# Performance work log

Measured on AMD Instinct MI355X. Metric: run time of the kernel, lower is better.

Reference implementation:

```python
import jax, jax.numpy as jnp
import numpy as np

EMBED = 1024
HEADS = 16
HEAD_DIM = EMBED // HEADS
WIN = 256  # attention_window w; band width = 2w+1


def setup_inputs() -> dict:
    key = jax.random.key(0)
    ks = jax.random.split(key, 10)
    b, s, e = 2, 4096, EMBED
    scale = 1.0 / np.sqrt(e)
    inp = {"x": jax.random.normal(ks[0], (b, s, e), jnp.float32)}
    for i, (wn, bn) in enumerate([("Wq", "bq"), ("Wk", "bk"), ("Wv", "bv"), ("Wo", "bo")]):
        inp[wn] = jax.random.normal(ks[1 + i], (e, e), jnp.float32) * scale
        inp[bn] = jax.random.normal(ks[5 + i], (e,), jnp.float32) * 0.01
    return inp


def _rope_headaxis(x):
    # Replicates RotaryEmbedding applied to [b, s, h, d]: the original indexes
    # x.shape[2] (== num_heads here), so phase varies over the HEAD axis.
    h, d = x.shape[2], x.shape[3]
    inv = 1.0 / (10000.0 ** (jnp.arange(0, d, 2, dtype=jnp.float32) / d))
    freqs = jnp.arange(h, dtype=jnp.float32)[:, None] * inv[None, :]
    emb = jnp.concatenate([freqs, freqs], axis=-1)  # [h, d]
    cos = jnp.cos(emb)[None, None]  # [1,1,h,d]
    sin = jnp.sin(emb)[None, None]
    x2 = jnp.stack([-x[..., 1::2], x[..., 0::2]], axis=-1).reshape(x.shape)
    return x * cos + x2 * sin


def reference(x, Wq, bq, Wk, bk, Wv, bv, Wo, bo):
    b, s, e = x.shape
    h, d, w = HEADS, HEAD_DIM, WIN
    q = (x @ Wq.T + bq).reshape(b, s, h, d)
    k = (x @ Wk.T + bk).reshape(b, s, h, d)
    v = (x @ Wv.T + bv).reshape(b, s, h, d)
    q = _rope_headaxis(q) / jnp.sqrt(jnp.float32(d))
    k = _rope_headaxis(k)

    # Band (sliding-window) attention: query chunk c of size w attends to key
    # chunks c-1, c, c+1 (3w keys); relative-position + boundary masking makes
    # this identical to the original sliding_chunks band of width 2w+1.
    nc = s // w
    qc = q.reshape(b, nc, w, h, d)
    pad = [(0, 0), (w, w), (0, 0), (0, 0)]
    kp = jnp.pad(k, pad)
    vp = jnp.pad(v, pad)
    idx = jnp.arange(nc)[:, None] * w + jnp.arange(3 * w)[None, :]  # [nc, 3w]
    k3 = kp[:, idx]  # [b, nc, 3w, h, d]
    v3 = vp[:, idx]
    scores = jnp.einsum('bcxhd,bcyhd->bhcxy', qc, k3)  # [b,h,nc,w,3w]

    c = jnp.arange(nc)[:, None, None]
    xq = jnp.arange(w)[None, :, None]
    y = jnp.arange(3 * w)[None, None, :]
    kpos = c * w + y - w  # absolute key position
    valid = (y >= xq) & (y <= xq + 2 * w) & (kpos >= 0) & (kpos < s)
    scores = jnp.where(valid[None, None], scores, -jnp.inf)

    probs = jax.nn.softmax(scores, axis=-1)  # fp32 softmax, as in original
    ctx = jnp.einsum('bhcxy,bcyhd->bcxhd', probs, v3).reshape(b, s, e)
    return ctx @ Wo.T + bo
```

## Files before the change

### kernel.cpp

```cpp
#include <hip/hip_runtime.h>


typedef _Float16 half8 __attribute__((ext_vector_type(8)));
typedef _Float16 half4v __attribute__((ext_vector_type(4)));
typedef float floatx4 __attribute__((ext_vector_type(4)));

typedef __attribute__((address_space(3))) unsigned int lds_u32;
typedef const __attribute__((address_space(1))) unsigned int glb_u32;

__device__ __forceinline__ void async_copy16(const void* g, void* l) {
  __builtin_amdgcn_global_load_lds((glb_u32*)g, (lds_u32*)l, 16, 0, 0);
}

__global__ __launch_bounds__(256) void convert_kernel(
    const float* __restrict__ x, const float* __restrict__ wq,
    const float* __restrict__ wk, const float* __restrict__ wv,
    const float* __restrict__ wo, _Float16* __restrict__ dst) {
  const int e0 = (blockIdx.x * 256 + threadIdx.x) * 4;
  const float* src; int off;
  if      (e0 <  8388608) { src = x;  off = e0; }
  else if (e0 <  9437184) { src = wq; off = e0 -  8388608; }
  else if (e0 < 10485760) { src = wk; off = e0 -  9437184; }
  else if (e0 < 11534336) { src = wv; off = e0 - 10485760; }
  else                    { src = wo; off = e0 - 11534336; }
  const float4 f = *(const float4*)(src + off);
  half4v h;
  h[0] = (_Float16)f.x; h[1] = (_Float16)f.y;
  h[2] = (_Float16)f.z; h[3] = (_Float16)f.w;
  *(half4v*)(dst + e0) = h;
}

__global__ __launch_bounds__(256, 2) void gemm_qkv_kernel(
    const _Float16* __restrict__ A, const _Float16* __restrict__ w0,
    const _Float16* __restrict__ w1, const _Float16* __restrict__ w2,
    const float* __restrict__ b0, const float* __restrict__ b1,
    const float* __restrict__ b2, _Float16* __restrict__ o0,
    _Float16* __restrict__ o1, _Float16* __restrict__ o2) {
  __shared__ _Float16 smem[17408];
  _Float16* As = smem;
  _Float16* Bs = smem + 8192;

  const int tid = threadIdx.x;
  const int w = tid >> 6, lane = tid & 63;
  const int l4 = lane & 15, quad = lane >> 4;
  const int wm = w & 1, wn = w >> 1;

  const int bid = blockIdx.x;
  const int xcd = bid & 7, li = bid >> 3;
  const int z = li >> 6, r_ = li & 63;
  const int n_l = r_ >> 3, m_l = r_ & 7;
  const int m0 = (xcd * 8 + m_l) * 128;
  const int n0 = n_l * 128;

  const _Float16* B; const float* bias; _Float16* out;
  if (z == 0)      { B = w0; bias = b0; out = o0; }
  else if (z == 1) { B = w1; bias = b1; out = o1; }
  else             { B = w2; bias = b2; out = o2; }
  const bool dorope = z < 2;
  const float scl = (z == 0) ? 0.18033688f : 1.0f;

  const floatx4 zero = {0.f, 0.f, 0.f, 0.f};
  floatx4 acc[4][4];
#pragma unroll
  for (int i = 0; i < 4; ++i)
#pragma unroll
    for (int j = 0; j < 4; ++j) acc[i][j] = zero;

  for (int kt = 0; kt < 16; ++kt) {
    const int k0 = kt * 64;
#pragma unroll
    for (int i = 0; i < 4; ++i) {
      const int p = i * 256 + tid;
      const int r = p >> 3;
      const int c = (p & 7) ^ (r & 7);
      async_copy16(A + (m0 + r) * 1024 + k0 + c * 8, As + (i * 256 + w * 64) * 8);
      async_copy16(B + (n0 + r) * 1024 + k0 + c * 8, Bs + (i * 256 + w * 64) * 8);
    }
    __syncthreads();
#pragma unroll
    for (int ks = 0; ks < 2; ++ks) {
      half8 af[4], bf[4];
#pragma unroll
      for (int mt = 0; mt < 4; ++mt)
        af[mt] = *(const half8*)(As + (wm * 64 + mt * 16 + l4) * 64 +
                                 (((ks * 4 + quad) ^ (l4 & 7)) * 8));
#pragma unroll
      for (int nt = 0; nt < 4; ++nt)
        bf[nt] = *(const half8*)(Bs + (wn * 64 + nt * 16 + l4) * 64 +
                                 (((ks * 4 + quad) ^ (l4 & 7)) * 8));
#pragma unroll
      for (int mt = 0; mt < 4; ++mt)
#pragma unroll
        for (int nt = 0; nt < 4; ++nt)
          acc[mt][nt] = __builtin_amdgcn_mfma_f32_16x16x32_f16(af[mt], bf[nt], acc[mt][nt], 0, 0, 0);
    }
    __syncthreads();
  }

  _Float16* tile = smem;
#pragma unroll
  for (int nt = 0; nt < 4; ++nt) {
    const int n = n0 + wn * 64 + nt * 16 + l4;
    const float bval = bias[n];
    const int hh = n >> 6;
    float c_ = 1.f, ss = 0.f;
    if (dorope) {
      const float freq = __expf((float)(n & 31) * -0.28782314f);
      float s_;
      __sincosf((float)hh * freq, &s_, &c_);
      ss = (n & 1) ? s_ : -s_;
    }
#pragma unroll
    for (int mt = 0; mt < 4; ++mt)
#pragma unroll
      for (int r = 0; r < 4; ++r) {
        float val = acc[mt][nt][r] + bval;
        const float prt = __shfl_xor(val, 1);
        if (dorope) val = (val * c_ + prt * ss) * scl;
        const int ml = wm * 64 + mt * 16 + quad * 4 + r;
        const int nl = wn * 64 + nt * 16 + l4;
        if (z == 2) tile[nl * 132 + ml] = (_Float16)val;
        else        tile[ml * 132 + nl] = (_Float16)val;
      }
  }
  __syncthreads();
  if (z == 2) {
#pragma unroll
    for (int j = 0; j < 8; ++j) {
      const int idx = j * 256 + tid;
      const int row = idx >> 4, cb = idx & 15;
      const int n = n0 + row, hh = n >> 6, dd = n & 63;
      const int m = m0 + cb * 8, bb = m >> 12, s = m & 4095;
      const half8 vals = *(const half8*)(tile + row * 132 + cb * 8);
      *(half8*)(out + (bb * 16 + hh) * 262144 + dd * 4096 + s) = vals;
    }
  } else {
#pragma unroll
    for (int j = 0; j < 8; ++j) {
      const int idx = j * 256 + tid;
      const int row = idx >> 4, cb = idx & 15;
      const int n = n0 + cb * 8, hh = n >> 6, dd = n & 63;
      const int m = m0 + row, bb = m >> 12, s = m & 4095;
      const half8 vals = *(const half8*)(tile + row * 132 + cb * 8);
      *(half8*)(out + ((bb * 16 + hh) * 4096 + s) * 64 + dd) = vals;
    }
  }
}

__global__ __launch_bounds__(256, 2) void gemm_out_kernel(
    const _Float16* __restrict__ A, const _Float16* __restrict__ B,
    const float* __restrict__ bias, float* __restrict__ out) {
  __shared__ _Float16 smem[16384];
  _Float16* As = smem;
  _Float16* Bs = smem + 8192;

  const int tid = threadIdx.x;
  const int w = tid >> 6, lane = tid & 63;
  const int l4 = lane & 15, quad = lane >> 4;
  const int wm = w & 1, wn = w >> 1;

  const int bid = blockIdx.x;
  const int xcd = bid & 7, li = bid >> 3;
  const int n_l = li >> 3, m_l = li & 7;
  const int m0 = (xcd * 8 + m_l) * 128;
  const int n0 = n_l * 128;

  const floatx4 zero = {0.f, 0.f, 0.f, 0.f};
  floatx4 acc[4][4];
#pragma unroll
  for (int i = 0; i < 4; ++i)
#pragma unroll
    for (int j = 0; j < 4; ++j) acc[i][j] = zero;

  for (int kt = 0; kt < 16; ++kt) {
    const int k0 = kt * 64;
#pragma unroll
    for (int i = 0; i < 4; ++i) {
      const int p = i * 256 + tid;
      const int r = p >> 3;
      const int c = (p & 7) ^ (r & 7);
      async_copy16(A + (m0 + r) * 1024 + k0 + c * 8, As + (i * 256 + w * 64) * 8);
      async_copy16(B + (n0 + r) * 1024 + k0 + c * 8, Bs + (i * 256 + w * 64) * 8);
    }
    __syncthreads();
#pragma unroll
    for (int ks = 0; ks < 2; ++ks) {
      half8 af[4], bf[4];
#pragma unroll
      for (int mt = 0; mt < 4; ++mt)
        af[mt] = *(const half8*)(As + (wm * 64 + mt * 16 + l4) * 64 +
                                 (((ks * 4 + quad) ^ (l4 & 7)) * 8));
#pragma unroll
      for (int nt = 0; nt < 4; ++nt)
        bf[nt] = *(const half8*)(Bs + (wn * 64 + nt * 16 + l4) * 64 +
                                 (((ks * 4 + quad) ^ (l4 & 7)) * 8));
#pragma unroll
      for (int mt = 0; mt < 4; ++mt)
#pragma unroll
        for (int nt = 0; nt < 4; ++nt)
          acc[mt][nt] = __builtin_amdgcn_mfma_f32_16x16x32_f16(af[mt], bf[nt], acc[mt][nt], 0, 0, 0);
    }
    __syncthreads();
  }

#pragma unroll
  for (int nt = 0; nt < 4; ++nt) {
    const int n = n0 + wn * 64 + nt * 16 + l4;
    const float bval = bias[n];
#pragma unroll
    for (int mt = 0; mt < 4; ++mt)
#pragma unroll
      for (int r = 0; r < 4; ++r) {
        const int m = m0 + wm * 64 + mt * 16 + quad * 4 + r;
        out[m * 1024 + n] = acc[mt][nt][r] + bval;
      }
  }
}

__global__ __launch_bounds__(256, 2) void attn_kernel(
    const _Float16* __restrict__ qg, const _Float16* __restrict__ kg,
    const _Float16* __restrict__ vtg, _Float16* __restrict__ ctx) {
  __shared__ _Float16 Ks[128 * 64];
  __shared__ _Float16 Vs[64 * 128];

  const int tid = threadIdx.x;
  const int w = tid >> 6, lane = tid & 63;
  const int l4 = lane & 15, quad = lane >> 4;
  const int q0 = blockIdx.x * 256;
  const int bh = blockIdx.y;
  const _Float16* qbh = qg + bh * 262144;
  const _Float16* kbh = kg + bh * 262144;
  const _Float16* vbh = vtg + bh * 262144;

  half8 qf[2][2][2];
#pragma unroll
  for (int sub = 0; sub < 2; ++sub)
#pragma unroll
    for (int nt = 0; nt < 2; ++nt)
#pragma unroll
      for (int ks = 0; ks < 2; ++ks)
        qf[sub][nt][ks] = *(const half8*)(qbh + (q0 + sub * 128 + w * 32 + nt * 16 + l4) * 64 +
                                          ks * 32 + quad * 8);

  const floatx4 zero = {0.f, 0.f, 0.f, 0.f};
  floatx4 OT[2][4][2];
  float l_st[2][2];
#pragma unroll
  for (int sub = 0; sub < 2; ++sub) {
#pragma unroll
    for (int md = 0; md < 4; ++md)
#pragma unroll
      for (int nt = 0; nt < 2; ++nt) OT[sub][md][nt] = zero;
#pragma unroll
    for (int nt = 0; nt < 2; ++nt) l_st[sub][nt] = 0.f;
  }

  for (int t = 0; t < 6; ++t) {
    const int kv0 = q0 - 256 + t * 128;
    if (kv0 < 0 || kv0 >= 4096) continue;

#pragma unroll
    for (int i = 0; i < 4; ++i) {
      const int p = i * 256 + tid;
      const int rk = p >> 3, ck = (p & 7) ^ (rk & 7);
      async_copy16(kbh + (kv0 + rk) * 64 + ck * 8, Ks + (i * 256 + w * 64) * 8);
      const int rv = p >> 4, cv = (p & 15) ^ (rv & 7);
      async_copy16(vbh + rv * 4096 + kv0 + cv * 8, Vs + (i * 256 + w * 64) * 8);
    }
    __syncthreads();

#pragma unroll
    for (int sub = 0; sub < 2; ++sub) {
      if ((t == 0 && sub == 1) || (t == 5 && sub == 0)) continue;
      const bool needmask = (t == 0 && sub == 0) || (t == 1 && sub == 1) ||
                            (t == 4 && sub == 0) || (t == 5 && sub == 1);
      const int qbase = q0 + sub * 128 + w * 32;

#pragma unroll
      for (int hf = 0; hf < 2; ++hf) {
        const int kb = hf * 64;

        floatx4 ST[4][2];
#pragma unroll
        for (int m = 0; m < 4; ++m)
#pragma unroll
          for (int nt = 0; nt < 2; ++nt) ST[m][nt] = zero;
#pragma unroll
        for (int ks = 0; ks < 2; ++ks)
#pragma unroll
          for (int m = 0; m < 4; ++m) {
            const half8 kf = *(const half8*)(Ks + (kb + m * 16 + l4) * 64 +
                                             ((ks * 4 + quad) ^ (l4 & 7)) * 8);
#pragma unroll
            for (int nt = 0; nt < 2; ++nt)
              ST[m][nt] = __builtin_amdgcn_mfma_f32_16x16x32_f16(kf, qf[sub][nt][ks], ST[m][nt], 0, 0, 0);
          }

        if (needmask) {
#pragma unroll
          for (int m = 0; m < 4; ++m)
#pragma unroll
            for (int r = 0; r < 4; ++r) {
              const int key = kv0 + kb + m * 16 + quad * 4 + r;
#pragma unroll
              for (int nt = 0; nt < 2; ++nt) {
                const int d = key - (qbase + nt * 16 + l4);
                if (d < -256 || d > 256) ST[m][nt][r] = -1e30f;
              }
            }
        }

#pragma unroll
        for (int nt = 0; nt < 2; ++nt) {
          float rs = 0.f;
#pragma unroll
          for (int m = 0; m < 4; ++m)
#pragma unroll
            for (int r = 0; r < 4; ++r) {
              const float pv = exp2f(ST[m][nt][r] - 4.0f);
              ST[m][nt][r] = pv;
              rs += pv;
            }
          l_st[sub][nt] += rs;
        }

#pragma unroll
        for (int m = 0; m < 4; ++m) {
          half4v pb[2];
#pragma unroll
          for (int nt = 0; nt < 2; ++nt) {
            const auto lo = __builtin_amdgcn_cvt_pkrtz(ST[m][nt][0], ST[m][nt][1]);
            const auto hi = __builtin_amdgcn_cvt_pkrtz(ST[m][nt][2], ST[m][nt][3]);
            pb[nt][0] = (_Float16)lo[0]; pb[nt][1] = (_Float16)lo[1];
            pb[nt][2] = (_Float16)hi[0]; pb[nt][3] = (_Float16)hi[1];
          }
#pragma unroll
          for (int md = 0; md < 4; ++md) {
            const half4v vf = *(const half4v*)(Vs + (md * 16 + l4) * 128 +
                                               (((hf * 8 + m * 2 + (quad >> 1)) ^ (l4 & 7)) * 8 +
                                                (quad & 1) * 4));
#pragma unroll
            for (int nt = 0; nt < 2; ++nt)
              OT[sub][md][nt] = __builtin_amdgcn_mfma_f32_16x16x16f16(vf, pb[nt], OT[sub][md][nt], 0, 0, 0);
          }
        }
      }
    }
    __syncthreads();
  }

  const int b = bh >> 4, hh = bh & 15;
#pragma unroll
  for (int sub = 0; sub < 2; ++sub)
#pragma unroll
    for (int nt = 0; nt < 2; ++nt) {
      float lt = l_st[sub][nt];
      lt += __shfl_xor(lt, 16);
      lt += __shfl_xor(lt, 32);
      const float inv_l = 1.f / lt;
      const int s = q0 + sub * 128 + w * 32 + nt * 16 + l4;
#pragma unroll
      for (int md = 0; md < 4; ++md) {
        half4v o;
#pragma unroll
        for (int r = 0; r < 4; ++r) o[r] = (_Float16)(OT[sub][md][nt][r] * inv_l);
        *(half4v*)(ctx + (b * 4096 + s) * 1024 + hh * 64 + md * 16 + quad * 4) = o;
      }
    }
}

extern "C" void kernel_launch(void* const* d_in, const int* in_sizes, int n_in,
                              void* d_out, int out_size, void* d_ws, size_t ws_size,
                              hipStream_t stream) {
  const float* x  = (const float*)d_in[0];
  const float* Wq = (const float*)d_in[1];
  const float* bq = (const float*)d_in[2];
  const float* Wk = (const float*)d_in[3];
  const float* bk = (const float*)d_in[4];
  const float* Wv = (const float*)d_in[5];
  const float* bv = (const float*)d_in[6];
  const float* Wo = (const float*)d_in[7];
  const float* bo = (const float*)d_in[8];

  _Float16* ws   = (_Float16*)d_ws;
  _Float16* xh   = ws;
  _Float16* wqh  = ws + 8388608;
  _Float16* wkh  = ws + 9437184;
  _Float16* wvh  = ws + 10485760;
  _Float16* woh  = ws + 11534336;
  _Float16* qh   = ws + 12582912;
  _Float16* kh   = ws + 20971520;
  _Float16* vth  = ws + 29360128;
  _Float16* ctxh = xh;

  convert_kernel<<<12288, 256, 0, stream>>>(x, Wq, Wk, Wv, Wo, ws);
  gemm_qkv_kernel<<<1536, 256, 0, stream>>>(xh, wqh, wkh, wvh,
                                            bq, bk, bv, qh, kh, vth);
  attn_kernel<<<dim3(16, 32), 256, 0, stream>>>(qh, kh, vth, ctxh);
  gemm_out_kernel<<<512, 256, 0, stream>>>(ctxh, woh, bo, (float*)d_out);
}
```

Baseline: 232.6 us.

## Use 256x128 GEMM tiles with triple-buffered async loads and split MFMA phases

Replaces both GEMM main loops with a shared routine that computes 256x128 tiles (BK=32) using a three-stage LDS ring of async global->LDS loads, explicit vmcnt waits, and s_setprio around MFMA bursts. Grid sizes halve and each wave accumulates 8x4 fragments, raising arithmetic intensity and overlapping loads with compute. The QKV epilogue is split into two 128-row halves to reuse LDS for the transposed writes. Costs are more registers and LDS (72KB per block), which may limit occupancy, and fewer blocks relative to CU count.

```diff
diff --git a/kernel.cpp b/kernel.cpp
--- a/kernel.cpp
+++ b/kernel.cpp
@@ -30,15 +30,113 @@
   *(half4v*)(dst + e0) = h;
 }
 
+__device__ __forceinline__ void gemm256_mainloop(
+    const _Float16* __restrict__ Ag, const _Float16* __restrict__ Bg,
+    _Float16* smem, const int m0, const int n0, floatx4 (&acc)[8][4]) {
+  const int tid = threadIdx.x;
+  const int w = tid >> 6, lane = tid & 63;
+  const int l4 = lane & 15, quad = lane >> 4;
+  const int wm = w & 1, wn = w >> 1;
+
+  int srcA[4], srcB[2];
+#pragma unroll
+  for (int i = 0; i < 4; ++i) {
+    const int p = i * 256 + tid;
+    const int r = p >> 2;
+    const int g = (p & 3) ^ ((r >> 1) & 3);
+    srcA[i] = (m0 + r) * 1024 + g * 8;
+  }
+#pragma unroll
+  for (int i = 0; i < 2; ++i) {
+    const int p = i * 256 + tid;
+    const int r = p >> 2;
+    const int g = (p & 3) ^ ((r >> 1) & 3);
+    srcB[i] = (n0 + r) * 1024 + g * 8;
+  }
+  const int dstw = w * 512;
+
+  const int swz = (quad ^ ((l4 >> 1) & 3)) * 8;
+  const int a_off = (wm * 128 + l4) * 32 + swz;
+  const int b_off = (wn * 64 + l4) * 32 + swz;
+
+  const floatx4 zero = {0.f, 0.f, 0.f, 0.f};
+#pragma unroll
+  for (int i = 0; i < 8; ++i)
+#pragma unroll
+    for (int j = 0; j < 4; ++j) acc[i][j] = zero;
+
+  auto stage = [&](int bufbase, int kt, int ph) {
+    _Float16* Ad = smem + bufbase;
+    _Float16* Bd = Ad + 8192;
+    const int k0 = kt * 32;
+    if (ph == 0) {
+      async_copy16(Ag + srcA[0] + k0, Ad + dstw);
+      async_copy16(Ag + srcA[1] + k0, Ad + 2048 + dstw);
+      async_copy16(Bg + srcB[0] + k0, Bd + dstw);
+    } else {
+      async_copy16(Ag + srcA[2] + k0, Ad + 4096 + dstw);
+      async_copy16(Ag + srcA[3] + k0, Ad + 6144 + dstw);
+      async_copy16(Bg + srcB[1] + k0, Bd + 2048 + dstw);
+    }
+  };
+
+  stage(0, 0, 0);     stage(0, 0, 1);
+  stage(12288, 1, 0); stage(12288, 1, 1);
+
+  int cb_ = 0, nb_ = 24576;
+  for (int t = 0; t < 32; ++t) {
+    _Float16* Ac = smem + cb_;
+    _Float16* Bc = Ac + 8192;
+
+    if (t < 30) {
+      stage(nb_, t + 2, 0);
+      asm volatile("s_waitcnt vmcnt(9)" ::: "memory");
+    } else if (t == 30) {
+      asm volatile("s_waitcnt vmcnt(6)" ::: "memory");
+    } else {
+      asm volatile("s_waitcnt vmcnt(0)" ::: "memory");
+    }
+    __builtin_amdgcn_s_barrier();
+
+    half8 af[4], bf[4];
+#pragma unroll
+    for (int mt = 0; mt < 4; ++mt) af[mt] = *(const half8*)(Ac + a_off + mt * 512);
+#pragma unroll
+    for (int nt = 0; nt < 4; ++nt) bf[nt] = *(const half8*)(Bc + b_off + nt * 512);
+    __builtin_amdgcn_s_setprio(1);
+#pragma unroll
+    for (int mt = 0; mt < 4; ++mt)
+#pragma unroll
+      for (int nt = 0; nt < 4; ++nt)
+        acc[mt][nt] = __builtin_amdgcn_mfma_f32_16x16x32_f16(af[mt], bf[nt], acc[mt][nt], 0, 0, 0);
+    __builtin_amdgcn_s_setprio(0);
+    __builtin_amdgcn_s_barrier();
+
+#pragma unroll
+    for (int mt = 0; mt < 4; ++mt) af[mt] = *(const half8*)(Ac + a_off + (mt + 4) * 512);
+    if (t < 30) stage(nb_, t + 2, 1);
+    __builtin_amdgcn_s_barrier();
+    __builtin_amdgcn_s_setprio(1);
+#pragma unroll
+    for (int mt = 0; mt < 4; ++mt)
+#pragma unroll
+      for (int nt = 0; nt < 4; ++nt)
+        acc[mt + 4][nt] = __builtin_amdgcn_mfma_f32_16x16x32_f16(af[mt], bf[nt], acc[mt + 4][nt], 0, 0, 0);
+    __builtin_amdgcn_s_setprio(0);
+    __builtin_amdgcn_s_barrier();
+
+    cb_ += 12288; if (cb_ == 36864) cb_ = 0;
+    nb_ += 12288; if (nb_ == 36864) nb_ = 0;
+  }
+}
+
 __global__ __launch_bounds__(256, 2) void gemm_qkv_kernel(
     const _Float16* __restrict__ A, const _Float16* __restrict__ w0,
     const _Float16* __restrict__ w1, const _Float16* __restrict__ w2,
     const float* __restrict__ b0, const float* __restrict__ b1,
     const float* __restrict__ b2, _Float16* __restrict__ o0,
     _Float16* __restrict__ o1, _Float16* __restrict__ o2) {
-  __shared__ _Float16 smem[17408];
-  _Float16* As = smem;
-  _Float16* Bs = smem + 8192;
+  __shared__ _Float16 smem[36864];
 
   const int tid = threadIdx.x;
   const int w = tid >> 6, lane = tid & 63;
@@ -47,10 +145,9 @@
 
   const int bid = blockIdx.x;
   const int xcd = bid & 7, li = bid >> 3;
-  const int z = li >> 6, r_ = li & 63;
-  const int n_l = r_ >> 3, m_l = r_ & 7;
-  const int m0 = (xcd * 8 + m_l) * 128;
-  const int n0 = n_l * 128;
+  const int z = li >> 5, li_z = li & 31;
+  const int m0 = (xcd * 4 + (li_z & 3)) * 256;
+  const int n0 = (li_z >> 2) * 128;
 
   const _Float16* B; const float* bias; _Float16* out;
   if (z == 0)      { B = w0; bias = b0; out = o0; }
@@ -59,100 +156,71 @@
   const bool dorope = z < 2;
   const float scl = (z == 0) ? 0.18033688f : 1.0f;
 
-  const floatx4 zero = {0.f, 0.f, 0.f, 0.f};
-  floatx4 acc[4][4];
-#pragma unroll
-  for (int i = 0; i < 4; ++i)
-#pragma unroll
-    for (int j = 0; j < 4; ++j) acc[i][j] = zero;
-
-  for (int kt = 0; kt < 16; ++kt) {
-    const int k0 = kt * 64;
-#pragma unroll
-    for (int i = 0; i < 4; ++i) {
-      const int p = i * 256 + tid;
-      const int r = p >> 3;
-      const int c = (p & 7) ^ (r & 7);
-      async_copy16(A + (m0 + r) * 1024 + k0 + c * 8, As + (i * 256 + w * 64) * 8);
-      async_copy16(B + (n0 + r) * 1024 + k0 + c * 8, Bs + (i * 256 + w * 64) * 8);
+  floatx4 acc[8][4];
+  gemm256_mainloop(A, B, smem, m0, n0, acc);
+
+  _Float16* tile = smem;
+  for (int h = 0; h < 2; ++h) {
+    if (wm == h) {
+#pragma unroll
+      for (int nt = 0; nt < 4; ++nt) {
+        const int n = n0 + wn * 64 + nt * 16 + l4;
+        const float bval = bias[n];
+        const int hh = n >> 6;
+        float c_ = 1.f, ss = 0.f;
+        if (dorope) {
+          const float freq = __expf((float)(n & 31) * -0.28782314f);
+          float s_;
+          __sincosf((float)hh * freq, &s_, &c_);
+          ss = (n & 1) ? s_ : -s_;
+        }
+#pragma unroll
+        for (int mt = 0; mt < 8; ++mt)
+#pragma unroll
+          for (int r = 0; r < 4; ++r) {
+            float val = acc[mt][nt][r] + bval;
+            const float prt = __shfl_xor(val, 1);
+            if (dorope) val = (val * c_ + prt * ss) * scl;
+            const int ml = mt * 16 + quad * 4 + r;
+            const int nl = wn * 64 + nt * 16 + l4;
+            if (z == 2) tile[nl * 132 + ml] = (_Float16)val;
+            else        tile[ml * 132 + nl] = (_Float16)val;
+          }
+      }
     }
     __syncthreads();
-#pragma unroll
-    for (int ks = 0; ks < 2; ++ks) {
-      half8 af[4], bf[4];
-#pragma unroll
-      for (int mt = 0; mt < 4; ++mt)
-        af[mt] = *(const half8*)(As + (wm * 64 + mt * 16 + l4) * 64 +
-                                 (((ks * 4 + quad) ^ (l4 & 7)) * 8));
-#pragma unroll
-      for (int nt = 0; nt < 4; ++nt)
-        bf[nt] = *(const half8*)(Bs + (wn * 64 + nt * 16 + l4) * 64 +
-                                 (((ks * 4 + quad) ^ (l4 & 7)) * 8));
-#pragma unroll
-      for (int mt = 0; mt < 4; ++mt)
-#pragma unroll
-        for (int nt = 0; nt < 4; ++nt)
-          acc[mt][nt] = __builtin_amdgcn_mfma_f32_16x16x32_f16(af[mt], bf[nt], acc[mt][nt], 0, 0, 0);
+
+    const int mg = m0 + h * 128;
+    const int bb = mg >> 12, sg = mg & 4095;
+    if (z == 2) {
+#pragma unroll
+      for (int tt = 0; tt < 8; ++tt) {
+        const int idx = tt * 256 + tid;
+        const int rr = idx >> 4, cbk = idx & 15;
+        const int n = n0 + rr, hh2 = n >> 6, dd = n & 63;
+        const int s = sg + cbk * 8;
+        const half8 vals = *(const half8*)(tile + rr * 132 + cbk * 8);
+        *(half8*)(out + (bb * 16 + hh2) * 262144 + dd * 4096 + s) = vals;
+      }
+    } else {
+#pragma unroll
+      for (int tt = 0; tt < 8; ++tt) {
+        const int idx = tt * 256 + tid;
+        const int rr = idx >> 4, cbk = idx & 15;
+        const int n = n0 + cbk * 8, hh2 = n >> 6, dd = n & 63;
+        const int s = sg + rr;
+        const half8 vals = *(const half8*)(tile + rr * 132 + cbk * 8);
+        *(half8*)(out + ((bb * 16 + hh2) * 4096 + s) * 64 + dd) = vals;
+      }
     }
     __syncthreads();
-  }
-
-  _Float16* tile = smem;
-#pragma unroll
-  for (int nt = 0; nt < 4; ++nt) {
-    const int n = n0 + wn * 64 + nt * 16 + l4;
-    const float bval = bias[n];
-    const int hh = n >> 6;
-    float c_ = 1.f, ss = 0.f;
-    if (dorope) {
-      const float freq = __expf((float)(n & 31) * -0.28782314f);
-      float s_;
-      __sincosf((float)hh * freq, &s_, &c_);
-      ss = (n & 1) ? s_ : -s_;
-    }
-#pragma unroll
-    for (int mt = 0; mt < 4; ++mt)
-#pragma unroll
-      for (int r = 0; r < 4; ++r) {
-        float val = acc[mt][nt][r] + bval;
-        const float prt = __shfl_xor(val, 1);
-        if (dorope) val = (val * c_ + prt * ss) * scl;
-        const int ml = wm * 64 + mt * 16 + quad * 4 + r;
-        const int nl = wn * 64 + nt * 16 + l4;
-        if (z == 2) tile[nl * 132 + ml] = (_Float16)val;
-        else        tile[ml * 132 + nl] = (_Float16)val;
-      }
-  }
-  __syncthreads();
-  if (z == 2) {
-#pragma unroll
-    for (int j = 0; j < 8; ++j) {
-      const int idx = j * 256 + tid;
-      const int row = idx >> 4, cb = idx & 15;
-      const int n = n0 + row, hh = n >> 6, dd = n & 63;
-      const int m = m0 + cb * 8, bb = m >> 12, s = m & 4095;
-      const half8 vals = *(const half8*)(tile + row * 132 + cb * 8);
-      *(half8*)(out + (bb * 16 + hh) * 262144 + dd * 4096 + s) = vals;
-    }
-  } else {
-#pragma unroll
-    for (int j = 0; j < 8; ++j) {
-      const int idx = j * 256 + tid;
-      const int row = idx >> 4, cb = idx & 15;
-      const int n = n0 + cb * 8, hh = n >> 6, dd = n & 63;
-      const int m = m0 + row, bb = m >> 12, s = m & 4095;
-      const half8 vals = *(const half8*)(tile + row * 132 + cb * 8);
-      *(half8*)(out + ((bb * 16 + hh) * 4096 + s) * 64 + dd) = vals;
-    }
   }
 }
 
 __global__ __launch_bounds__(256, 2) void gemm_out_kernel(
     const _Float16* __restrict__ A, const _Float16* __restrict__ B,
     const float* __restrict__ bias, float* __restrict__ out) {
-  __shared__ _Float16 smem[16384];
-  _Float16* As = smem;
-  _Float16* Bs = smem + 8192;
+  __shared__ _Float16 smem[36864];
 
   const int tid = threadIdx.x;
   const int w = tid >> 6, lane = tid & 63;
@@ -161,57 +229,21 @@
 
   const int bid = blockIdx.x;
   const int xcd = bid & 7, li = bid >> 3;
-  const int n_l = li >> 3, m_l = li & 7;
-  const int m0 = (xcd * 8 + m_l) * 128;
-  const int n0 = n_l * 128;
-
-  const floatx4 zero = {0.f, 0.f, 0.f, 0.f};
-  floatx4 acc[4][4];
-#pragma unroll
-  for (int i = 0; i < 4; ++i)
-#pragma unroll
-    for (int j = 0; j < 4; ++j) acc[i][j] = zero;
-
-  for (int kt = 0; kt < 16; ++kt) {
-    const int k0 = kt * 64;
-#pragma unroll
-    for (int i = 0; i < 4; ++i) {
-      const int p = i * 256 + tid;
-      const int r = p >> 3;
-      const int c = (p & 7) ^ (r & 7);
-      async_copy16(A + (m0 + r) * 1024 + k0 + c * 8, As + (i * 256 + w * 64) * 8);
-      async_copy16(B + (n0 + r) * 1024 + k0 + c * 8, Bs + (i * 256 + w * 64) * 8);
-    }
-    __syncthreads();
-#pragma unroll
-    for (int ks = 0; ks < 2; ++ks) {
-      half8 af[4], bf[4];
-#pragma unroll
-      for (int mt = 0; mt < 4; ++mt)
-        af[mt] = *(const half8*)(As + (wm * 64 + mt * 16 + l4) * 64 +
-                                 (((ks * 4 + quad) ^ (l4 & 7)) * 8));
-#pragma unroll
-      for (int nt = 0; nt < 4; ++nt)
-        bf[nt] = *(const half8*)(Bs + (wn * 64 + nt * 16 + l4) * 64 +
-                                 (((ks * 4 + quad) ^ (l4 & 7)) * 8));
-#pragma unroll
-      for (int mt = 0; mt < 4; ++mt)
-#pragma unroll
-        for (int nt = 0; nt < 4; ++nt)
-          acc[mt][nt] = __builtin_amdgcn_mfma_f32_16x16x32_f16(af[mt], bf[nt], acc[mt][nt], 0, 0, 0);
-    }
-    __syncthreads();
-  }
+  const int m0 = (xcd * 4 + (li & 3)) * 256;
+  const int n0 = (li >> 2) * 128;
+
+  floatx4 acc[8][4];
+  gemm256_mainloop(A, B, smem, m0, n0, acc);
 
 #pragma unroll
   for (int nt = 0; nt < 4; ++nt) {
     const int n = n0 + wn * 64 + nt * 16 + l4;
     const float bval = bias[n];
 #pragma unroll
-    for (int mt = 0; mt < 4; ++mt)
+    for (int mt = 0; mt < 8; ++mt)
 #pragma unroll
       for (int r = 0; r < 4; ++r) {
-        const int m = m0 + wm * 64 + mt * 16 + quad * 4 + r;
+        const int m = m0 + wm * 128 + mt * 16 + quad * 4 + r;
         out[m * 1024 + n] = acc[mt][nt][r] + bval;
       }
   }
@@ -394,8 +426,8 @@
   _Float16* ctxh = xh;
 
   convert_kernel<<<12288, 256, 0, stream>>>(x, Wq, Wk, Wv, Wo, ws);
-  gemm_qkv_kernel<<<1536, 256, 0, stream>>>(xh, wqh, wkh, wvh,
-                                            bq, bk, bv, qh, kh, vth);
+  gemm_qkv_kernel<<<768, 256, 0, stream>>>(xh, wqh, wkh, wvh,
+                                           bq, bk, bv, qh, kh, vth);
   attn_kernel<<<dim3(16, 32), 256, 0, stream>>>(qh, kh, vth, ctxh);
-  gemm_out_kernel<<<512, 256, 0, stream>>>(ctxh, woh, bo, (float*)d_out);
-}
+  gemm_out_kernel<<<256, 256, 0, stream>>>(ctxh, woh, bo, (float*)d_out);
+}
```

New measurement: 258.1 us. +11.0%, slower.

## Halve attention query tile, swizzle block order, skip out-of-band key halves

Applied to the files above, without the earlier changes.

Each attention block now handles 128 queries instead of 256, doubling the grid to 1024 one-dimensional blocks. Block indices are remapped so that adjacent blocks spread across batch-head pairs. Each warp skips 64-key halves entirely outside its band and masks only where needed. Smaller per-block register state allows raising the occupancy hint to 4 blocks per CU. In exchange, each K/V tile staged in LDS is reused by fewer queries, so total K/V loads increase.

```diff
diff --git a/kernel.cpp b/kernel.cpp
--- a/kernel.cpp
+++ b/kernel.cpp
@@ -217,7 +217,7 @@
   }
 }
 
-__global__ __launch_bounds__(256, 2) void attn_kernel(
+__global__ __launch_bounds__(256, 4) void attn_kernel(
     const _Float16* __restrict__ qg, const _Float16* __restrict__ kg,
     const _Float16* __restrict__ vtg, _Float16* __restrict__ ctx) {
   __shared__ _Float16 Ks[128 * 64];
@@ -226,36 +226,35 @@
   const int tid = threadIdx.x;
   const int w = tid >> 6, lane = tid & 63;
   const int l4 = lane & 15, quad = lane >> 4;
-  const int q0 = blockIdx.x * 256;
-  const int bh = blockIdx.y;
+
+  const int bid = blockIdx.x;
+  const int li = bid >> 3;
+  const int bh = (bid & 7) * 4 + (li >> 5);
+  const int q0 = (li & 31) * 128;
+
   const _Float16* qbh = qg + bh * 262144;
   const _Float16* kbh = kg + bh * 262144;
   const _Float16* vbh = vtg + bh * 262144;
 
-  half8 qf[2][2][2];
-#pragma unroll
-  for (int sub = 0; sub < 2; ++sub)
-#pragma unroll
-    for (int nt = 0; nt < 2; ++nt)
-#pragma unroll
-      for (int ks = 0; ks < 2; ++ks)
-        qf[sub][nt][ks] = *(const half8*)(qbh + (q0 + sub * 128 + w * 32 + nt * 16 + l4) * 64 +
-                                          ks * 32 + quad * 8);
+  half8 qf[2][2];
+#pragma unroll
+  for (int nt = 0; nt < 2; ++nt)
+#pragma unroll
+    for (int ks = 0; ks < 2; ++ks)
+      qf[nt][ks] = *(const half8*)(qbh + (q0 + w * 32 + nt * 16 + l4) * 64 +
+                                   ks * 32 + quad * 8);
 
   const floatx4 zero = {0.f, 0.f, 0.f, 0.f};
-  floatx4 OT[2][4][2];
-  float l_st[2][2];
-#pragma unroll
-  for (int sub = 0; sub < 2; ++sub) {
-#pragma unroll
-    for (int md = 0; md < 4; ++md)
-#pragma unroll
-      for (int nt = 0; nt < 2; ++nt) OT[sub][md][nt] = zero;
-#pragma unroll
-    for (int nt = 0; nt < 2; ++nt) l_st[sub][nt] = 0.f;
-  }
-
-  for (int t = 0; t < 6; ++t) {
+  floatx4 OT[4][2];
+  float l_st[2] = {0.f, 0.f};
+#pragma unroll
+  for (int md = 0; md < 4; ++md)
+#pragma unroll
+    for (int nt = 0; nt < 2; ++nt) OT[md][nt] = zero;
+
+  const int qbase = q0 + w * 32;
+
+  for (int t = 0; t < 5; ++t) {
     const int kv0 = q0 - 256 + t * 128;
     if (kv0 < 0 || kv0 >= 4096) continue;
 
@@ -270,80 +269,75 @@
     __syncthreads();
 
 #pragma unroll
-    for (int sub = 0; sub < 2; ++sub) {
-      if ((t == 0 && sub == 1) || (t == 5 && sub == 0)) continue;
-      const bool needmask = (t == 0 && sub == 0) || (t == 1 && sub == 1) ||
-                            (t == 4 && sub == 0) || (t == 5 && sub == 1);
-      const int qbase = q0 + sub * 128 + w * 32;
-
-#pragma unroll
-      for (int hf = 0; hf < 2; ++hf) {
-        const int kb = hf * 64;
-
-        floatx4 ST[4][2];
+    for (int hf = 0; hf < 2; ++hf) {
+      const int kb = hf * 64;
+      const int k_lo = kv0 + kb, k_hi = k_lo + 63;
+      if (k_lo - (qbase + 31) > 256 || k_hi - qbase < -256) continue;
+      const bool needm = (k_lo - (qbase + 31) < -256) || (k_hi - qbase > 256);
+
+      floatx4 ST[4][2];
+#pragma unroll
+      for (int m = 0; m < 4; ++m)
+#pragma unroll
+        for (int nt = 0; nt < 2; ++nt) ST[m][nt] = zero;
+#pragma unroll
+      for (int ks = 0; ks < 2; ++ks)
+#pragma unroll
+        for (int m = 0; m < 4; ++m) {
+          const half8 kf = *(const half8*)(Ks + (kb + m * 16 + l4) * 64 +
+                                           ((ks * 4 + quad) ^ (l4 & 7)) * 8);
+#pragma unroll
+          for (int nt = 0; nt < 2; ++nt)
+            ST[m][nt] = __builtin_amdgcn_mfma_f32_16x16x32_f16(kf, qf[nt][ks], ST[m][nt], 0, 0, 0);
+        }
+
+      if (needm) {
 #pragma unroll
         for (int m = 0; m < 4; ++m)
 #pragma unroll
-          for (int nt = 0; nt < 2; ++nt) ST[m][nt] = zero;
-#pragma unroll
-        for (int ks = 0; ks < 2; ++ks)
-#pragma unroll
-          for (int m = 0; m < 4; ++m) {
-            const half8 kf = *(const half8*)(Ks + (kb + m * 16 + l4) * 64 +
-                                             ((ks * 4 + quad) ^ (l4 & 7)) * 8);
-#pragma unroll
-            for (int nt = 0; nt < 2; ++nt)
-              ST[m][nt] = __builtin_amdgcn_mfma_f32_16x16x32_f16(kf, qf[sub][nt][ks], ST[m][nt], 0, 0, 0);
+          for (int r = 0; r < 4; ++r) {
+            const int key = kv0 + kb + m * 16 + quad * 4 + r;
+#pragma unroll
+            for (int nt = 0; nt < 2; ++nt) {
+              const int d = key - (qbase + nt * 16 + l4);
+              if (d < -256 || d > 256) ST[m][nt][r] = -1e30f;
+            }
           }
-
-        if (needmask) {
-#pragma unroll
-          for (int m = 0; m < 4; ++m)
-#pragma unroll
-            for (int r = 0; r < 4; ++r) {
-              const int key = kv0 + kb + m * 16 + quad * 4 + r;
-#pragma unroll
-              for (int nt = 0; nt < 2; ++nt) {
-                const int d = key - (qbase + nt * 16 + l4);
-                if (d < -256 || d > 256) ST[m][nt][r] = -1e30f;
-              }
-            }
+      }
+
+#pragma unroll
+      for (int nt = 0; nt < 2; ++nt) {
+        float rs = 0.f;
+#pragma unroll
+        for (int m = 0; m < 4; ++m)
+#pragma unroll
+          for (int r = 0; r < 4; ++r) {
+            const float pv = exp2f(ST[m][nt][r] - 4.0f);
+            ST[m][nt][r] = pv;
+            rs += pv;
+          }
+        l_st[nt] += rs;
+      }
+
+#pragma unroll
+      for (int m = 0; m < 4; ++m) {
+        half4v pb[2];
+#pragma unroll
+        for (int nt = 0; nt < 2; ++nt) {
+          const auto lo = __builtin_amdgcn_cvt_pkrtz(ST[m][nt][0], ST[m][nt][1]);
+          const auto hi = __builtin_amdgcn_cvt_pkrtz(ST[m][nt][2], ST[m][nt][3]);
+          pb[nt][0] = (_Float16)lo[0]; pb[nt][1] = (_Float16)lo[1];
+          pb[nt][2] = (_Float16)hi[0]; pb[nt][3] = (_Float16)hi[1];
         }
-
-#pragma unroll
-        for (int nt = 0; nt < 2; ++nt) {
-          float rs = 0.f;
-#pragma unroll
-          for (int m = 0; m < 4; ++m)
-#pragma unroll
-            for (int r = 0; r < 4; ++r) {
-              const float pv = exp2f(ST[m][nt][r] - 4.0f);
-              ST[m][nt][r] = pv;
-              rs += pv;
-            }
-          l_st[sub][nt] += rs;
+#pragma unroll
+        for (int md = 0; md < 4; ++md) {
+          const half4v vf = *(const half4v*)(Vs + (md * 16 + l4) * 128 +
+                                             (((hf * 8 + m * 2 + (quad >> 1)) ^ (l4 & 7)) * 8 +
+                                              (quad & 1) * 4));
+#pragma unroll
+          for (int nt = 0; nt < 2; ++nt)
+            OT[md][nt] = __builtin_amdgcn_mfma_f32_16x16x16f16(vf, pb[nt], OT[md][nt], 0, 0, 0);
         }
-
-#pragma unroll
-        for (int m = 0; m < 4; ++m) {
-          half4v pb[2];
-#pragma unroll
-          for (int nt = 0; nt < 2; ++nt) {
-            const auto lo = __builtin_amdgcn_cvt_pkrtz(ST[m][nt][0], ST[m][nt][1]);
-            const auto hi = __builtin_amdgcn_cvt_pkrtz(ST[m][nt][2], ST[m][nt][3]);
-            pb[nt][0] = (_Float16)lo[0]; pb[nt][1] = (_Float16)lo[1];
-            pb[nt][2] = (_Float16)hi[0]; pb[nt][3] = (_Float16)hi[1];
-          }
-#pragma unroll
-          for (int md = 0; md < 4; ++md) {
-            const half4v vf = *(const half4v*)(Vs + (md * 16 + l4) * 128 +
-                                               (((hf * 8 + m * 2 + (quad >> 1)) ^ (l4 & 7)) * 8 +
-                                                (quad & 1) * 4));
-#pragma unroll
-            for (int nt = 0; nt < 2; ++nt)
-              OT[sub][md][nt] = __builtin_amdgcn_mfma_f32_16x16x16f16(vf, pb[nt], OT[sub][md][nt], 0, 0, 0);
-          }
-        }
       }
     }
     __syncthreads();
@@ -351,22 +345,20 @@
 
   const int b = bh >> 4, hh = bh & 15;
 #pragma unroll
-  for (int sub = 0; sub < 2; ++sub)
-#pragma unroll
-    for (int nt = 0; nt < 2; ++nt) {
-      float lt = l_st[sub][nt];
-      lt += __shfl_xor(lt, 16);
-      lt += __shfl_xor(lt, 32);
-      const float inv_l = 1.f / lt;
-      const int s = q0 + sub * 128 + w * 32 + nt * 16 + l4;
-#pragma unroll
-      for (int md = 0; md < 4; ++md) {
-        half4v o;
-#pragma unroll
-        for (int r = 0; r < 4; ++r) o[r] = (_Float16)(OT[sub][md][nt][r] * inv_l);
-        *(half4v*)(ctx + (b * 4096 + s) * 1024 + hh * 64 + md * 16 + quad * 4) = o;
-      }
-    }
+  for (int nt = 0; nt < 2; ++nt) {
+    float lt = l_st[nt];
+    lt += __shfl_xor(lt, 16);
+    lt += __shfl_xor(lt, 32);
+    const float inv_l = 1.f / lt;
+    const int s = q0 + w * 32 + nt * 16 + l4;
+#pragma unroll
+    for (int md = 0; md < 4; ++md) {
+      half4v o;
+#pragma unroll
+      for (int r = 0; r < 4; ++r) o[r] = (_Float16)(OT[md][nt][r] * inv_l);
+      *(half4v*)(ctx + (b * 4096 + s) * 1024 + hh * 64 + md * 16 + quad * 4) = o;
+    }
+  }
 }
 
 extern "C" void kernel_launch(void* const* d_in, const int* in_sizes, int n_in,
@@ -396,6 +388,6 @@
   convert_kernel<<<12288, 256, 0, stream>>>(x, Wq, Wk, Wv, Wo, ws);
   gemm_qkv_kernel<<<1536, 256, 0, stream>>>(xh, wqh, wkh, wvh,
                                             bq, bk, bv, qh, kh, vth);
-  attn_kernel<<<dim3(16, 32), 256, 0, stream>>>(qh, kh, vth, ctxh);
+  attn_kernel<<<1024, 256, 0, stream>>>(qh, kh, vth, ctxh);
   gemm_out_kernel<<<512, 256, 0, stream>>>(ctxh, woh, bo, (float*)d_out);
 }
```

Measured after the change: 253.5 us. +9.0%, slower.

## Double-buffer K/V tiles in attention and remap blocks to XCDs

Applied to the files above, without the earlier changes.

The attention kernel now double-buffers its K and V shared-memory tiles, issuing async loads for the next 128-key tile before computing the current one and using vmcnt waits instead of full syncthreads. Block indices are remapped so that all query tiles of a batch-head land on the same XCD, improving L2 reuse of the K/V data. Per-wave tile skipping and masking are now derived from the actual key range rather than fixed per-t flags, which skips out-of-band 64-key halves. Doubling the LDS usage to 64KB may reduce occupancy under launch bounds of 2 blocks per CU.

```diff
diff --git a/kernel.cpp b/kernel.cpp
--- a/kernel.cpp
+++ b/kernel.cpp
@@ -220,14 +220,18 @@
 __global__ __launch_bounds__(256, 2) void attn_kernel(
     const _Float16* __restrict__ qg, const _Float16* __restrict__ kg,
     const _Float16* __restrict__ vtg, _Float16* __restrict__ ctx) {
-  __shared__ _Float16 Ks[128 * 64];
-  __shared__ _Float16 Vs[64 * 128];
+  __shared__ _Float16 Ks[2][128 * 64];
+  __shared__ _Float16 Vs[2][64 * 128];
 
   const int tid = threadIdx.x;
   const int w = tid >> 6, lane = tid & 63;
   const int l4 = lane & 15, quad = lane >> 4;
-  const int q0 = blockIdx.x * 256;
-  const int bh = blockIdx.y;
+
+  const int bid = blockIdx.x;
+  const int xcd = bid & 7, li = bid >> 3;
+  const int bh = xcd * 4 + (li >> 4);
+  const int q0 = (li & 15) * 256;
+
   const _Float16* qbh = qg + bh * 262144;
   const _Float16* kbh = kg + bh * 262144;
   const _Float16* vbh = vtg + bh * 262144;
@@ -255,30 +259,43 @@
     for (int nt = 0; nt < 2; ++nt) l_st[sub][nt] = 0.f;
   }
 
-  for (int t = 0; t < 6; ++t) {
-    const int kv0 = q0 - 256 + t * 128;
-    if (kv0 < 0 || kv0 >= 4096) continue;
-
+  const int tb = (q0 == 0) ? 2 : 0;
+  const int te = (q0 == 3840) ? 3 : 5;
+
+  auto stage = [&](int b_, int kv0_) {
 #pragma unroll
     for (int i = 0; i < 4; ++i) {
       const int p = i * 256 + tid;
       const int rk = p >> 3, ck = (p & 7) ^ (rk & 7);
-      async_copy16(kbh + (kv0 + rk) * 64 + ck * 8, Ks + (i * 256 + w * 64) * 8);
+      async_copy16(kbh + (kv0_ + rk) * 64 + ck * 8, &Ks[b_][(i * 256 + w * 64) * 8]);
       const int rv = p >> 4, cv = (p & 15) ^ (rv & 7);
-      async_copy16(vbh + rv * 4096 + kv0 + cv * 8, Vs + (i * 256 + w * 64) * 8);
-    }
-    __syncthreads();
+      async_copy16(vbh + rv * 4096 + kv0_ + cv * 8, &Vs[b_][(i * 256 + w * 64) * 8]);
+    }
+  };
+
+  stage(tb & 1, q0 - 256 + tb * 128);
+
+  for (int t = tb; t <= te; ++t) {
+    const int kv0 = q0 - 256 + t * 128;
+    if (t < te) {
+      stage((t + 1) & 1, kv0 + 128);
+      asm volatile("s_waitcnt vmcnt(8)" ::: "memory");
+    } else {
+      asm volatile("s_waitcnt vmcnt(0)" ::: "memory");
+    }
+    __builtin_amdgcn_s_barrier();
+    const _Float16* Kc = Ks[t & 1];
+    const _Float16* Vc = Vs[t & 1];
 
 #pragma unroll
     for (int sub = 0; sub < 2; ++sub) {
-      if ((t == 0 && sub == 1) || (t == 5 && sub == 0)) continue;
-      const bool needmask = (t == 0 && sub == 0) || (t == 1 && sub == 1) ||
-                            (t == 4 && sub == 0) || (t == 5 && sub == 1);
       const int qbase = q0 + sub * 128 + w * 32;
-
 #pragma unroll
       for (int hf = 0; hf < 2; ++hf) {
         const int kb = hf * 64;
+        const int k_lo = kv0 + kb, k_hi = k_lo + 63;
+        if (k_lo - (qbase + 31) > 256 || k_hi - qbase < -256) continue;
+        const bool needm = (k_lo - (qbase + 31) < -256) || (k_hi - qbase > 256);
 
         floatx4 ST[4][2];
 #pragma unroll
@@ -289,14 +306,14 @@
         for (int ks = 0; ks < 2; ++ks)
 #pragma unroll
           for (int m = 0; m < 4; ++m) {
-            const half8 kf = *(const half8*)(Ks + (kb + m * 16 + l4) * 64 +
+            const half8 kf = *(const half8*)(Kc + (kb + m * 16 + l4) * 64 +
                                              ((ks * 4 + quad) ^ (l4 & 7)) * 8);
 #pragma unroll
             for (int nt = 0; nt < 2; ++nt)
               ST[m][nt] = __builtin_amdgcn_mfma_f32_16x16x32_f16(kf, qf[sub][nt][ks], ST[m][nt], 0, 0, 0);
           }
 
-        if (needmask) {
+        if (needm) {
 #pragma unroll
           for (int m = 0; m < 4; ++m)
 #pragma unroll
@@ -336,7 +353,7 @@
           }
 #pragma unroll
           for (int md = 0; md < 4; ++md) {
-            const half4v vf = *(const half4v*)(Vs + (md * 16 + l4) * 128 +
+            const half4v vf = *(const half4v*)(Vc + (md * 16 + l4) * 128 +
                                                (((hf * 8 + m * 2 + (quad >> 1)) ^ (l4 & 7)) * 8 +
                                                 (quad & 1) * 4));
 #pragma unroll
@@ -346,7 +363,12 @@
         }
       }
     }
-    __syncthreads();
+
+    if (t < te) {
+      asm volatile("s_waitcnt lgkmcnt(0)" ::: "memory");
+      __builtin_amdgcn_sched_barrier(0);
+      __builtin_amdgcn_s_barrier();
+    }
   }
 
   const int b = bh >> 4, hh = bh & 15;
@@ -396,6 +418,6 @@
   convert_kernel<<<12288, 256, 0, stream>>>(x, Wq, Wk, Wv, Wo, ws);
   gemm_qkv_kernel<<<1536, 256, 0, stream>>>(xh, wqh, wkh, wvh,
                                             bq, bk, bv, qh, kh, vth);
-  attn_kernel<<<dim3(16, 32), 256, 0, stream>>>(qh, kh, vth, ctxh);
+  attn_kernel<<<512, 256, 0, stream>>>(qh, kh, vth, ctxh);
   gemm_out_kernel<<<512, 256, 0, stream>>>(ctxh, woh, bo, (float*)d_out);
 }
```

New measurement: 227.9 us, median of 2. 1.02x faster.
